# Kernel optimization log

Hardware: AMD Instinct MI355X
Metric: run time of the kernel (lower is better)

## Reference

```python
import jax, jax.numpy as jnp
import numpy as np

K = 3  # from init kwarg


def setup_inputs() -> dict:
    key = jax.random.key(0)
    k1, k2 = jax.random.split(key)
    B, N, D = 32, 2048, 128
    features = jax.random.normal(k1, (B, N, D), dtype=jnp.float32)
    strength = jax.random.uniform(k2, (), dtype=jnp.float32)
    return {"features": features, "strength": strength}


def reference(features, strength):
    B, N, D = features.shape
    k = min(K, N - 1)
    x = jax.lax.stop_gradient(features)  # torch uses features.detach() for the mix path

    # pairwise euclidean distance (torch.cdist, p=2): ||a||^2 + ||b||^2 - 2 a.b
    sq = jnp.sum(x * x, axis=-1)                     # (B, N)
    d2 = sq[:, :, None] + sq[:, None, :] - 2.0 * jnp.einsum('bnd,bmd->bnm', x, x)
    dist = jnp.sqrt(jnp.maximum(d2, 0.0))            # (B, N, N)

    # mask self-distance with +1e6 on the diagonal
    eye = jnp.eye(N, dtype=dist.dtype)
    dist = dist + eye[None, :, :] * 1000000.0

    # k smallest -> top_k of negated distances
    _, idx = jax.lax.top_k(-dist, k)                 # idx: (B, N, k)

    # gather neighbor features: gathered[b,n,j] = x[b, idx[b,n,j]]
    gathered = x[jnp.arange(B)[:, None, None], idx]  # (B, N, k, D)
    mix = jnp.mean(gathered, axis=2)                 # (B, N, D)

    s = jnp.clip(strength, 0.0, 1.0)
    return (1.0 - s) * features + s * mix
```

## Files before the change

### kernel.cpp

```cpp
#include <hip/hip_runtime.h>
#include <cfloat>

#define BB 32
#define NN 2048
#define DD 128
#define RM 128
#define CN 64

typedef __attribute__((ext_vector_type(8))) short short8;
typedef __attribute__((ext_vector_type(4))) short short4v;
typedef __attribute__((ext_vector_type(4))) float float4v;

__device__ __forceinline__ unsigned short f2bf(float f) {
    unsigned int u = __builtin_bit_cast(unsigned int, f);
    u += 0x7FFFu + ((u >> 16) & 1u);
    return (unsigned short)(u >> 16);
}

__device__ __forceinline__ unsigned int umn(unsigned int a, unsigned int b) { return a < b ? a : b; }
__device__ __forceinline__ unsigned int umx(unsigned int a, unsigned int b) { return a > b ? a : b; }
#define CSU(a, b) { unsigned int _lo = umn(a, b), _hi = umx(a, b); (a) = _lo; (b) = _hi; }

__device__ __forceinline__ unsigned int umed3(unsigned int a, unsigned int b, unsigned int c) {
    unsigned int d;
    asm("v_med3_u32 %0, %1, %2, %3" : "=v"(d) : "v"(a), "v"(b), "v"(c));
    return d;
}

__device__ __forceinline__ void gl2lds16(const unsigned short* g, unsigned short* l) {
    __builtin_amdgcn_global_load_lds(
        (const __attribute__((address_space(1))) void*)g,
        (__attribute__((address_space(3))) void*)l, 16, 0, 0);
}

__global__ __launch_bounds__(256) void prep_kernel(const float* __restrict__ x,
        unsigned short* __restrict__ xb16, float* __restrict__ sq) {
    int c = blockIdx.x * 256 + threadIdx.x;
    float4 v = *reinterpret_cast<const float4*>(x + (size_t)c * 4);
    short4v pk;
    pk[0] = (short)f2bf(v.x); pk[1] = (short)f2bf(v.y);
    pk[2] = (short)f2bf(v.z); pk[3] = (short)f2bf(v.w);
    *reinterpret_cast<short4v*>(xb16 + (size_t)c * 4) = pk;
    float acc = v.x * v.x + v.y * v.y + v.z * v.z + v.w * v.w;
    acc += __shfl_xor(acc, 1);
    acc += __shfl_xor(acc, 2);
    acc += __shfl_xor(acc, 4);
    acc += __shfl_xor(acc, 8);
    acc += __shfl_xor(acc, 16);
    if ((threadIdx.x & 31) == 0) sq[c >> 5] = acc;
}

__global__ __launch_bounds__(256) void sq_kernel(const float* __restrict__ x,
                                                 float* __restrict__ sq) {
    int t = blockIdx.x * 256 + threadIdx.x;
    int row = t >> 2;
    int q = t & 3;
    const float4* xp = reinterpret_cast<const float4*>(x + (size_t)row * DD + q * 32);
    float acc = 0.f;
#pragma unroll
    for (int i = 0; i < 8; ++i) {
        float4 v = xp[i];
        acc += v.x * v.x + v.y * v.y + v.z * v.z + v.w * v.w;
    }
    acc += __shfl_xor(acc, 1);
    acc += __shfl_xor(acc, 2);
    if (q == 0) sq[row] = acc;
}

template<bool PRE>
__global__ __launch_bounds__(256, 2) void knn_kernel(const float* __restrict__ x,
        const unsigned short* __restrict__ xb16g,
        const float* __restrict__ sqv, const float* __restrict__ strength,
        float* __restrict__ out) {
    __shared__ __align__(16) unsigned short btile[2 * CN * DD];
    __shared__ unsigned int cand8[RM * 8];

    const int b = blockIdx.x;
    const int row0 = blockIdx.y * RM;
    const int tid = threadIdx.x;
    const int w = tid >> 6;
    const int lane = tid & 63;
    const int m = lane & 15;
    const int quad = lane >> 4;
    const float* __restrict__ xb = x + (size_t)b * NN * DD;
    const unsigned short* __restrict__ gb = PRE ? xb16g + (size_t)b * NN * DD : nullptr;

    short8 afrag[2][4];
    if constexpr (PRE) {
#pragma unroll
        for (int rg = 0; rg < 2; ++rg)
#pragma unroll
            for (int kc = 0; kc < 4; ++kc)
                afrag[rg][kc] = *reinterpret_cast<const short8*>(
                    gb + (size_t)(row0 + 32 * w + rg * 16 + m) * DD + kc * 32 + quad * 8);
    } else {
#pragma unroll
        for (int rg = 0; rg < 2; ++rg)
#pragma unroll
            for (int kc = 0; kc < 4; ++kc) {
                const float4* src = reinterpret_cast<const float4*>(
                    xb + (size_t)(row0 + 32 * w + rg * 16 + m) * DD + kc * 32 + quad * 8);
                float4 v0 = src[0], v1 = src[1];
                short8 pk;
                pk[0] = (short)f2bf(v0.x); pk[1] = (short)f2bf(v0.y);
                pk[2] = (short)f2bf(v0.z); pk[3] = (short)f2bf(v0.w);
                pk[4] = (short)f2bf(v1.x); pk[5] = (short)f2bf(v1.y);
                pk[6] = (short)f2bf(v1.z); pk[7] = (short)f2bf(v1.w);
                afrag[rg][kc] = pk;
            }
    }

    {
        unsigned short* buf = btile;
        if constexpr (PRE) {
#pragma unroll
            for (int l = 0; l < 4; ++l) {
                int f = (l * 4 + w) * 64 + lane;
                int r = f >> 4, p = f & 15;
                int c = p ^ (r & 7);
                gl2lds16(gb + (size_t)r * DD + c * 8, buf + (l * 4 + w) * 512);
            }
        } else {
#pragma unroll
            for (int l = 0; l < 4; ++l) {
                int id = l * 256 + tid;
                int r = id >> 4, c = id & 15, p = c ^ (r & 7);
                const float4* src = reinterpret_cast<const float4*>(xb + (size_t)r * DD + c * 8);
                float4 v0 = src[0], v1 = src[1];
                short8 pk;
                pk[0] = (short)f2bf(v0.x); pk[1] = (short)f2bf(v0.y);
                pk[2] = (short)f2bf(v0.z); pk[3] = (short)f2bf(v0.w);
                pk[4] = (short)f2bf(v1.x); pk[5] = (short)f2bf(v1.y);
                pk[6] = (short)f2bf(v1.z); pk[7] = (short)f2bf(v1.w);
                *reinterpret_cast<short8*>(buf + r * DD + p * 8) = pk;
            }
        }
    }
    __syncthreads();

    unsigned int tk[2][4][4];
#pragma unroll
    for (int rg = 0; rg < 2; ++rg)
#pragma unroll
        for (int i = 0; i < 4; ++i)
#pragma unroll
            for (int q = 0; q < 4; ++q) tk[rg][i][q] = 0xFFFFFFFFu;

    for (int ct = 0; ct < NN / CN; ++ct) {
        unsigned short* cur = btile + (size_t)(ct & 1) * CN * DD;
        unsigned short* nxt = btile + (size_t)((ct + 1) & 1) * CN * DD;

        if (ct + 1 < NN / CN) {
            int cb = (ct + 1) * CN;
            if constexpr (PRE) {
#pragma unroll
                for (int l = 0; l < 4; ++l) {
                    int f = (l * 4 + w) * 64 + lane;
                    int r = f >> 4, p = f & 15;
                    int c = p ^ (r & 7);
                    gl2lds16(gb + (size_t)(cb + r) * DD + c * 8, nxt + (l * 4 + w) * 512);
                }
            } else {
#pragma unroll
                for (int l = 0; l < 4; ++l) {
                    int id = l * 256 + tid;
                    int r = id >> 4, c = id & 15, p = c ^ (r & 7);
                    const float4* src = reinterpret_cast<const float4*>(xb + (size_t)(cb + r) * DD + c * 8);
                    float4 v0 = src[0], v1 = src[1];
                    short8 pk;
                    pk[0] = (short)f2bf(v0.x); pk[1] = (short)f2bf(v0.y);
                    pk[2] = (short)f2bf(v0.z); pk[3] = (short)f2bf(v0.w);
                    pk[4] = (short)f2bf(v1.x); pk[5] = (short)f2bf(v1.y);
                    pk[6] = (short)f2bf(v1.z); pk[7] = (short)f2bf(v1.w);
                    *reinterpret_cast<short8*>(nxt + r * DD + p * 8) = pk;
                }
            }
        }

        float sqb[4];
#pragma unroll
        for (int cc = 0; cc < 4; ++cc)
            sqb[cc] = sqv[(size_t)b * NN + ct * CN + cc * 16 + m] + 1024.0f;

        float4v acc[2][4];
#pragma unroll
        for (int rg = 0; rg < 2; ++rg)
#pragma unroll
            for (int cc = 0; cc < 4; ++cc) acc[rg][cc] = (float4v){0.f, 0.f, 0.f, 0.f};
        __builtin_amdgcn_s_setprio(1);
#pragma unroll
        for (int kc = 0; kc < 4; ++kc) {
            short8 bfrag[4];
#pragma unroll
            for (int cc = 0; cc < 4; ++cc) {
                int rl = cc * 16 + m;
                int p = (kc * 4 + quad) ^ (m & 7);
                bfrag[cc] = *reinterpret_cast<const short8*>(cur + rl * DD + p * 8);
            }
#pragma unroll
            for (int rg = 0; rg < 2; ++rg)
#pragma unroll
                for (int cc = 0; cc < 4; ++cc)
                    acc[rg][cc] = __builtin_amdgcn_mfma_f32_16x16x32_bf16(
                        afrag[rg][kc], bfrag[cc], acc[rg][cc], 0, 0, 0);
        }
        __builtin_amdgcn_s_setprio(0);

#pragma unroll
        for (int cc = 0; cc < 4; ++cc) {
            unsigned int col = (unsigned int)(ct * CN + cc * 16 + m);
#pragma unroll
            for (int rg = 0; rg < 2; ++rg)
#pragma unroll
                for (int reg = 0; reg < 4; ++reg) {
                    float scb = fmaf(-2.f, acc[rg][cc][reg], sqb[cc]);
                    unsigned int key = (__builtin_bit_cast(unsigned int, scb) & 0xFFFFF800u) | col;
                    unsigned int t0 = tk[rg][reg][0], t1 = tk[rg][reg][1];
                    unsigned int t2 = tk[rg][reg][2], t3 = tk[rg][reg][3];
                    tk[rg][reg][0] = umn(t0, key);
                    tk[rg][reg][1] = umed3(t0, t1, key);
                    tk[rg][reg][2] = umed3(t1, t2, key);
                    tk[rg][reg][3] = umed3(t2, t3, key);
                }
        }

        __syncthreads();
    }

#pragma unroll
    for (int rg = 0; rg < 2; ++rg)
#pragma unroll
        for (int reg = 0; reg < 4; ++reg) {
            unsigned int e[8];
#pragma unroll
            for (int j = 0; j < 4; ++j) e[j] = tk[rg][reg][j];
#pragma unroll
            for (int j = 4; j < 8; ++j) e[j] = 0xFFFFFFFFu;
#pragma unroll
            for (int st = 0; st < 4; ++st) {
                int mask = 1 << st;
                unsigned int rv[8];
#pragma unroll
                for (int j = 0; j < 8; ++j)
                    rv[j] = (unsigned int)__shfl_xor((int)e[7 - j], mask, 64);
#pragma unroll
                for (int j = 0; j < 8; ++j) e[j] = umn(e[j], rv[j]);
                CSU(e[0], e[4]); CSU(e[1], e[5]); CSU(e[2], e[6]); CSU(e[3], e[7]);
                CSU(e[0], e[2]); CSU(e[1], e[3]); CSU(e[4], e[6]); CSU(e[5], e[7]);
                CSU(e[0], e[1]); CSU(e[2], e[3]); CSU(e[4], e[5]); CSU(e[6], e[7]);
            }
            if (m == 0) {
                int row = 32 * w + rg * 16 + quad * 4 + reg;
#pragma unroll
                for (int j = 0; j < 8; ++j) cand8[row * 8 + j] = e[j];
            }
        }
    __syncthreads();

    double* refd = reinterpret_cast<double*>(btile);
    int* best3 = reinterpret_cast<int*>(btile) + 2048;

    {
        int r = tid >> 1, h = tid & 1;
        int grow = row0 + r;
        int ci[4];
#pragma unroll
        for (int j = 0; j < 4; ++j) ci[j] = (int)(cand8[r * 8 + h * 4 + j] & 0x7FFu);
        const float* pr = xb + (size_t)grow * DD;
        const float* pc[4];
#pragma unroll
        for (int j = 0; j < 4; ++j) pc[j] = xb + (size_t)ci[j] * DD;
        double a[4] = {0.0, 0.0, 0.0, 0.0};
#pragma unroll 4
        for (int d4 = 0; d4 < 32; ++d4) {
            float4 wv = *reinterpret_cast<const float4*>(pr + d4 * 4);
#pragma unroll
            for (int j = 0; j < 4; ++j) {
                float4 v = *reinterpret_cast<const float4*>(pc[j] + d4 * 4);
                double d;
                d = (double)wv.x - (double)v.x; a[j] += d * d;
                d = (double)wv.y - (double)v.y; a[j] += d * d;
                d = (double)wv.z - (double)v.z; a[j] += d * d;
                d = (double)wv.w - (double)v.w; a[j] += d * d;
            }
        }
#pragma unroll
        for (int j = 0; j < 4; ++j)
            refd[r * 8 + h * 4 + j] = (ci[j] == grow) ? DBL_MAX : a[j];
    }
    __syncthreads();

    if (tid < RM) {
        int r = tid;
        double b0 = DBL_MAX, b1 = DBL_MAX, b2 = DBL_MAX;
        int i0 = 0x7fffffff, i1 = 0x7fffffff, i2 = 0x7fffffff;
        for (int e = 0; e < 8; ++e) {
            double dv = refd[r * 8 + e];
            int ix = (int)(cand8[r * 8 + e] & 0x7FFu);
            if (dv < b2 || (dv == b2 && ix < i2)) {
                b2 = dv; i2 = ix;
                if (b1 > b2 || (b1 == b2 && i1 > i2)) { double td = b1; b1 = b2; b2 = td; int tn = i1; i1 = i2; i2 = tn; }
                if (b0 > b1 || (b0 == b1 && i0 > i1)) { double td = b0; b0 = b1; b1 = td; int tn = i0; i0 = i1; i1 = tn; }
            }
        }
        best3[r * 3 + 0] = i0; best3[r * 3 + 1] = i1; best3[r * 3 + 2] = i2;
    }
    __syncthreads();

    {
        int r = tid >> 1, q = tid & 1;
        float s = fminf(fmaxf(strength[0], 0.f), 1.f);
        const float* pa = xb + (size_t)(row0 + r) * DD + q * 64;
        const float* p1 = xb + (size_t)best3[r * 3 + 0] * DD + q * 64;
        const float* p2 = xb + (size_t)best3[r * 3 + 1] * DD + q * 64;
        const float* p3 = xb + (size_t)best3[r * 3 + 2] * DD + q * 64;
        float* po = out + ((size_t)b * NN + row0 + r) * DD + q * 64;
#pragma unroll
        for (int l = 0; l < 16; ++l) {
            float4 a  = *reinterpret_cast<const float4*>(pa + l * 4);
            float4 n1 = *reinterpret_cast<const float4*>(p1 + l * 4);
            float4 n2 = *reinterpret_cast<const float4*>(p2 + l * 4);
            float4 n3 = *reinterpret_cast<const float4*>(p3 + l * 4);
            float4 o;
            o.x = (1.f - s) * a.x + s * ((n1.x + n2.x + n3.x) / 3.f);
            o.y = (1.f - s) * a.y + s * ((n1.y + n2.y + n3.y) / 3.f);
            o.z = (1.f - s) * a.z + s * ((n1.z + n2.z + n3.z) / 3.f);
            o.w = (1.f - s) * a.w + s * ((n1.w + n2.w + n3.w) / 3.f);
            *reinterpret_cast<float4*>(po + l * 4) = o;
        }
    }
}

extern "C" void kernel_launch(void* const* d_in, const int* in_sizes, int n_in,
                              void* d_out, int out_size, void* d_ws, size_t ws_size,
                              hipStream_t stream) {
    const float* x = (const float*)d_in[0];
    const float* strength = (const float*)d_in[1];
    float* out = (float*)d_out;
    float* sq = (float*)d_ws;
    unsigned short* xb16 = (unsigned short*)((char*)d_ws + 256 * 1024);
    const size_t need = 256 * 1024 + (size_t)BB * NN * DD * sizeof(unsigned short);

    if (ws_size >= need) {
        prep_kernel<<<dim3((BB * NN * DD / 4) / 256), 256, 0, stream>>>(x, xb16, sq);
        knn_kernel<true><<<dim3(BB, NN / RM), 256, 0, stream>>>(x, xb16, sq, strength, out);
    } else {
        sq_kernel<<<dim3((BB * NN * 4) / 256), 256, 0, stream>>>(x, sq);
        knn_kernel<false><<<dim3(BB, NN / RM), 256, 0, stream>>>(x, nullptr, sq, strength, out);
    }
}
```

Measured before the change: 193.4 us.

## Triple-buffer B tiles with explicit vmcnt waits and prefetch squared norms

Moves the LDS B-tile pipeline from double to triple buffering, so the async global-to-LDS copy for tile ct+2 is issued while tile ct is being computed. The full __syncthreads is replaced by a partial s_waitcnt vmcnt(4) plus s_barrier, which leaves the newest prefetch in flight. Squared norms for the next tile are loaded one iteration early, and the setprio hints around the MFMA block are removed. The cost is 16KB more LDS per block, which may reduce occupancy, and hand-written waitcnt logic that depends on how the compiler orders memory operations.

```diff
diff --git a/kernel.cpp b/kernel.cpp
--- a/kernel.cpp
+++ b/kernel.cpp
@@ -6,6 +6,7 @@
 #define DD 128
 #define RM 128
 #define CN 64
+#define NT (NN / CN)
 
 typedef __attribute__((ext_vector_type(8))) short short8;
 typedef __attribute__((ext_vector_type(4))) short short4v;
@@ -72,7 +73,7 @@
         const unsigned short* __restrict__ xb16g,
         const float* __restrict__ sqv, const float* __restrict__ strength,
         float* __restrict__ out) {
-    __shared__ __align__(16) unsigned short btile[2 * CN * DD];
+    __shared__ __align__(16) unsigned short btile[3 * CN * DD];
     __shared__ unsigned int cand8[RM * 8];
 
     const int b = blockIdx.x;
@@ -110,32 +111,44 @@
             }
     }
 
-    {
-        unsigned short* buf = btile;
-        if constexpr (PRE) {
-#pragma unroll
-            for (int l = 0; l < 4; ++l) {
-                int f = (l * 4 + w) * 64 + lane;
-                int r = f >> 4, p = f & 15;
-                int c = p ^ (r & 7);
-                gl2lds16(gb + (size_t)r * DD + c * 8, buf + (l * 4 + w) * 512);
-            }
-        } else {
-#pragma unroll
-            for (int l = 0; l < 4; ++l) {
-                int id = l * 256 + tid;
-                int r = id >> 4, c = id & 15, p = c ^ (r & 7);
-                const float4* src = reinterpret_cast<const float4*>(xb + (size_t)r * DD + c * 8);
-                float4 v0 = src[0], v1 = src[1];
-                short8 pk;
-                pk[0] = (short)f2bf(v0.x); pk[1] = (short)f2bf(v0.y);
-                pk[2] = (short)f2bf(v0.z); pk[3] = (short)f2bf(v0.w);
-                pk[4] = (short)f2bf(v1.x); pk[5] = (short)f2bf(v1.y);
-                pk[6] = (short)f2bf(v1.z); pk[7] = (short)f2bf(v1.w);
-                *reinterpret_cast<short8*>(buf + r * DD + p * 8) = pk;
-            }
-        }
-    }
+    unsigned short* cur = btile;
+    unsigned short* n1  = btile + CN * DD;
+    unsigned short* n2  = btile + 2 * CN * DD;
+
+    if constexpr (PRE) {
+#pragma unroll
+        for (int l = 0; l < 4; ++l) {
+            int f = (l * 4 + w) * 64 + lane;
+            int r = f >> 4, p = f & 15;
+            int c = p ^ (r & 7);
+            gl2lds16(gb + (size_t)r * DD + c * 8, cur + (l * 4 + w) * 512);
+        }
+#pragma unroll
+        for (int l = 0; l < 4; ++l) {
+            int f = (l * 4 + w) * 64 + lane;
+            int r = f >> 4, p = f & 15;
+            int c = p ^ (r & 7);
+            gl2lds16(gb + (size_t)(CN + r) * DD + c * 8, n1 + (l * 4 + w) * 512);
+        }
+    } else {
+#pragma unroll
+        for (int l = 0; l < 8; ++l) {
+            int id = l * 256 + tid;
+            int r = id >> 4, c = id & 15, p = c ^ (r & 7);
+            const float4* src = reinterpret_cast<const float4*>(xb + (size_t)r * DD + c * 8);
+            float4 v0 = src[0], v1 = src[1];
+            short8 pk;
+            pk[0] = (short)f2bf(v0.x); pk[1] = (short)f2bf(v0.y);
+            pk[2] = (short)f2bf(v0.z); pk[3] = (short)f2bf(v0.w);
+            pk[4] = (short)f2bf(v1.x); pk[5] = (short)f2bf(v1.y);
+            pk[6] = (short)f2bf(v1.z); pk[7] = (short)f2bf(v1.w);
+            *reinterpret_cast<short8*>(btile + r * DD + p * 8) = pk;
+        }
+    }
+    float sqb[4];
+#pragma unroll
+    for (int cc = 0; cc < 4; ++cc)
+        sqb[cc] = sqv[(size_t)b * NN + cc * 16 + m] + 1024.0f;
     __syncthreads();
 
     unsigned int tk[2][4][4];
@@ -146,19 +159,25 @@
 #pragma unroll
             for (int q = 0; q < 4; ++q) tk[rg][i][q] = 0xFFFFFFFFu;
 
-    for (int ct = 0; ct < NN / CN; ++ct) {
-        unsigned short* cur = btile + (size_t)(ct & 1) * CN * DD;
-        unsigned short* nxt = btile + (size_t)((ct + 1) & 1) * CN * DD;
-
-        if (ct + 1 < NN / CN) {
-            int cb = (ct + 1) * CN;
+#pragma unroll 1
+    for (int ct = 0; ct < NT; ++ct) {
+        float sqn[4];
+        if (ct + 1 < NT) {
+#pragma unroll
+            for (int cc = 0; cc < 4; ++cc)
+                sqn[cc] = sqv[(size_t)b * NN + (ct + 1) * CN + cc * 16 + m];
+        }
+        asm volatile("" ::: "memory");
+
+        if (ct + 2 < NT) {
+            int cb = (ct + 2) * CN;
             if constexpr (PRE) {
 #pragma unroll
                 for (int l = 0; l < 4; ++l) {
                     int f = (l * 4 + w) * 64 + lane;
                     int r = f >> 4, p = f & 15;
                     int c = p ^ (r & 7);
-                    gl2lds16(gb + (size_t)(cb + r) * DD + c * 8, nxt + (l * 4 + w) * 512);
+                    gl2lds16(gb + (size_t)(cb + r) * DD + c * 8, n2 + (l * 4 + w) * 512);
                 }
             } else {
 #pragma unroll
@@ -172,22 +191,16 @@
                     pk[2] = (short)f2bf(v0.z); pk[3] = (short)f2bf(v0.w);
                     pk[4] = (short)f2bf(v1.x); pk[5] = (short)f2bf(v1.y);
                     pk[6] = (short)f2bf(v1.z); pk[7] = (short)f2bf(v1.w);
-                    *reinterpret_cast<short8*>(nxt + r * DD + p * 8) = pk;
+                    *reinterpret_cast<short8*>(n2 + r * DD + p * 8) = pk;
                 }
             }
         }
 
-        float sqb[4];
-#pragma unroll
-        for (int cc = 0; cc < 4; ++cc)
-            sqb[cc] = sqv[(size_t)b * NN + ct * CN + cc * 16 + m] + 1024.0f;
-
         float4v acc[2][4];
 #pragma unroll
         for (int rg = 0; rg < 2; ++rg)
 #pragma unroll
             for (int cc = 0; cc < 4; ++cc) acc[rg][cc] = (float4v){0.f, 0.f, 0.f, 0.f};
-        __builtin_amdgcn_s_setprio(1);
 #pragma unroll
         for (int kc = 0; kc < 4; ++kc) {
             short8 bfrag[4];
@@ -204,7 +217,6 @@
                     acc[rg][cc] = __builtin_amdgcn_mfma_f32_16x16x32_bf16(
                         afrag[rg][kc], bfrag[cc], acc[rg][cc], 0, 0, 0);
         }
-        __builtin_amdgcn_s_setprio(0);
 
 #pragma unroll
         for (int cc = 0; cc < 4; ++cc) {
@@ -224,7 +236,24 @@
                 }
         }
 
-        __syncthreads();
+        if (ct + 1 < NT) {
+#pragma unroll
+            for (int cc = 0; cc < 4; ++cc) sqb[cc] = sqn[cc] + 1024.0f;
+        }
+
+        if constexpr (PRE) {
+            if (ct + 2 < NT) {
+                asm volatile("s_waitcnt vmcnt(4)" ::: "memory");
+            } else {
+                asm volatile("s_waitcnt vmcnt(0)" ::: "memory");
+            }
+            __builtin_amdgcn_s_barrier();
+            __builtin_amdgcn_sched_barrier(0);
+        } else {
+            __syncthreads();
+        }
+
+        unsigned short* t = cur; cur = n1; n1 = n2; n2 = t;
     }
 
 #pragma unroll
@@ -318,14 +347,14 @@
 #pragma unroll
         for (int l = 0; l < 16; ++l) {
             float4 a  = *reinterpret_cast<const float4*>(pa + l * 4);
-            float4 n1 = *reinterpret_cast<const float4*>(p1 + l * 4);
-            float4 n2 = *reinterpret_cast<const float4*>(p2 + l * 4);
-            float4 n3 = *reinterpret_cast<const float4*>(p3 + l * 4);
+            float4 v1 = *reinterpret_cast<const float4*>(p1 + l * 4);
+            float4 v2 = *reinterpret_cast<const float4*>(p2 + l * 4);
+            float4 v3 = *reinterpret_cast<const float4*>(p3 + l * 4);
             float4 o;
-            o.x = (1.f - s) * a.x + s * ((n1.x + n2.x + n3.x) / 3.f);
-            o.y = (1.f - s) * a.y + s * ((n1.y + n2.y + n3.y) / 3.f);
-            o.z = (1.f - s) * a.z + s * ((n1.z + n2.z + n3.z) / 3.f);
-            o.w = (1.f - s) * a.w + s * ((n1.w + n2.w + n3.w) / 3.f);
+            o.x = (1.f - s) * a.x + s * ((v1.x + v2.x + v3.x) / 3.f);
+            o.y = (1.f - s) * a.y + s * ((v1.y + v2.y + v3.y) / 3.f);
+            o.z = (1.f - s) * a.z + s * ((v1.z + v2.z + v3.z) / 3.f);
+            o.w = (1.f - s) * a.w + s * ((v1.w + v2.w + v3.w) / 3.f);
             *reinterpret_cast<float4*>(po + l * 4) = o;
         }
     }
```

Measured after the change: 186.2 us, median of 2. 3.7% less time.

## Deepen LDS tile pipeline to four buffers with prefetch distance two

Applied to the files above, without the earlier changes.

The column-tile loop now uses four LDS buffers and issues async global-to-LDS loads two tiles ahead instead of one. It waits with explicit vmcnt counts plus a raw barrier rather than a full syncthreads, and unrolls four tiles per iteration with precomputed LDS addresses. Squared norms are now prefetched one tile ahead, and the +1024 bias is folded into the prep kernels. The cost is doubled LDS use, which may reduce occupancy, and hand-tuned wait counts that are easy to get wrong.

```diff
diff --git a/kernel.cpp b/kernel.cpp
--- a/kernel.cpp
+++ b/kernel.cpp
@@ -6,6 +6,7 @@
 #define DD 128
 #define RM 128
 #define CN 64
+#define NT (NN / CN)
 
 typedef __attribute__((ext_vector_type(8))) short short8;
 typedef __attribute__((ext_vector_type(4))) short short4v;
@@ -47,7 +48,7 @@
     acc += __shfl_xor(acc, 4);
     acc += __shfl_xor(acc, 8);
     acc += __shfl_xor(acc, 16);
-    if ((threadIdx.x & 31) == 0) sq[c >> 5] = acc;
+    if ((threadIdx.x & 31) == 0) sq[c >> 5] = acc + 1024.0f;
 }
 
 __global__ __launch_bounds__(256) void sq_kernel(const float* __restrict__ x,
@@ -64,7 +65,7 @@
     }
     acc += __shfl_xor(acc, 1);
     acc += __shfl_xor(acc, 2);
-    if (q == 0) sq[row] = acc;
+    if (q == 0) sq[row] = acc + 1024.0f;
 }
 
 template<bool PRE>
@@ -72,7 +73,7 @@
         const unsigned short* __restrict__ xb16g,
         const float* __restrict__ sqv, const float* __restrict__ strength,
         float* __restrict__ out) {
-    __shared__ __align__(16) unsigned short btile[2 * CN * DD];
+    __shared__ __align__(16) unsigned short btile[4 * CN * DD];
     __shared__ unsigned int cand8[RM * 8];
 
     const int b = blockIdx.x;
@@ -110,32 +111,50 @@
             }
     }
 
-    {
-        unsigned short* buf = btile;
-        if constexpr (PRE) {
-#pragma unroll
-            for (int l = 0; l < 4; ++l) {
-                int f = (l * 4 + w) * 64 + lane;
-                int r = f >> 4, p = f & 15;
-                int c = p ^ (r & 7);
-                gl2lds16(gb + (size_t)r * DD + c * 8, buf + (l * 4 + w) * 512);
-            }
-        } else {
-#pragma unroll
-            for (int l = 0; l < 4; ++l) {
-                int id = l * 256 + tid;
-                int r = id >> 4, c = id & 15, p = c ^ (r & 7);
-                const float4* src = reinterpret_cast<const float4*>(xb + (size_t)r * DD + c * 8);
-                float4 v0 = src[0], v1 = src[1];
-                short8 pk;
-                pk[0] = (short)f2bf(v0.x); pk[1] = (short)f2bf(v0.y);
-                pk[2] = (short)f2bf(v0.z); pk[3] = (short)f2bf(v0.w);
-                pk[4] = (short)f2bf(v1.x); pk[5] = (short)f2bf(v1.y);
-                pk[6] = (short)f2bf(v1.z); pk[7] = (short)f2bf(v1.w);
-                *reinterpret_cast<short8*>(buf + r * DD + p * 8) = pk;
-            }
-        }
-    }
+    const unsigned short* gsl[4];
+    int ldo[4];
+    int str_[4], stc_[4], stp_[4];
+#pragma unroll
+    for (int l = 0; l < 4; ++l) {
+        int f = (l * 4 + w) * 64 + lane;
+        int r = f >> 4, p = f & 15;
+        int c = p ^ (r & 7);
+        str_[l] = r; stc_[l] = c; stp_[l] = p;
+        if constexpr (PRE) gsl[l] = gb + (size_t)r * DD + c * 8;
+        ldo[l] = (l * 4 + w) * 512;
+    }
+    int baddr[16];
+#pragma unroll
+    for (int kc = 0; kc < 4; ++kc)
+#pragma unroll
+        for (int cc = 0; cc < 4; ++cc)
+            baddr[kc * 4 + cc] =
+                ((cc * 16 + m) * DD + (((kc * 4 + quad) ^ (m & 7)) * 8)) * 2;
+    const float* __restrict__ sqp = sqv + (size_t)b * NN + m;
+
+    if constexpr (PRE) {
+#pragma unroll
+        for (int l = 0; l < 4; ++l) gl2lds16(gsl[l], btile + ldo[l]);
+#pragma unroll
+        for (int l = 0; l < 4; ++l) gl2lds16(gsl[l] + (1 << 13), btile + CN * DD + ldo[l]);
+    } else {
+#pragma unroll
+        for (int l = 0; l < 8; ++l) {
+            int id = l * 256 + tid;
+            int r = id >> 4, c = id & 15, p = c ^ (r & 7);
+            const float4* src = reinterpret_cast<const float4*>(xb + (size_t)r * DD + c * 8);
+            float4 v0 = src[0], v1 = src[1];
+            short8 pk;
+            pk[0] = (short)f2bf(v0.x); pk[1] = (short)f2bf(v0.y);
+            pk[2] = (short)f2bf(v0.z); pk[3] = (short)f2bf(v0.w);
+            pk[4] = (short)f2bf(v1.x); pk[5] = (short)f2bf(v1.y);
+            pk[6] = (short)f2bf(v1.z); pk[7] = (short)f2bf(v1.w);
+            *reinterpret_cast<short8*>(btile + r * DD + p * 8) = pk;
+        }
+    }
+    float sqb[4];
+#pragma unroll
+    for (int cc = 0; cc < 4; ++cc) sqb[cc] = sqp[cc * 16];
     __syncthreads();
 
     unsigned int tk[2][4][4];
@@ -146,86 +165,107 @@
 #pragma unroll
             for (int q = 0; q < 4; ++q) tk[rg][i][q] = 0xFFFFFFFFu;
 
-    for (int ct = 0; ct < NN / CN; ++ct) {
-        unsigned short* cur = btile + (size_t)(ct & 1) * CN * DD;
-        unsigned short* nxt = btile + (size_t)((ct + 1) & 1) * CN * DD;
-
-        if (ct + 1 < NN / CN) {
-            int cb = (ct + 1) * CN;
-            if constexpr (PRE) {
-#pragma unroll
-                for (int l = 0; l < 4; ++l) {
-                    int f = (l * 4 + w) * 64 + lane;
-                    int r = f >> 4, p = f & 15;
-                    int c = p ^ (r & 7);
-                    gl2lds16(gb + (size_t)(cb + r) * DD + c * 8, nxt + (l * 4 + w) * 512);
-                }
-            } else {
-#pragma unroll
-                for (int l = 0; l < 4; ++l) {
-                    int id = l * 256 + tid;
-                    int r = id >> 4, c = id & 15, p = c ^ (r & 7);
-                    const float4* src = reinterpret_cast<const float4*>(xb + (size_t)(cb + r) * DD + c * 8);
-                    float4 v0 = src[0], v1 = src[1];
-                    short8 pk;
-                    pk[0] = (short)f2bf(v0.x); pk[1] = (short)f2bf(v0.y);
-                    pk[2] = (short)f2bf(v0.z); pk[3] = (short)f2bf(v0.w);
-                    pk[4] = (short)f2bf(v1.x); pk[5] = (short)f2bf(v1.y);
-                    pk[6] = (short)f2bf(v1.z); pk[7] = (short)f2bf(v1.w);
-                    *reinterpret_cast<short8*>(nxt + r * DD + p * 8) = pk;
-                }
-            }
-        }
-
-        float sqb[4];
-#pragma unroll
-        for (int cc = 0; cc < 4; ++cc)
-            sqb[cc] = sqv[(size_t)b * NN + ct * CN + cc * 16 + m] + 1024.0f;
-
-        float4v acc[2][4];
-#pragma unroll
-        for (int rg = 0; rg < 2; ++rg)
-#pragma unroll
-            for (int cc = 0; cc < 4; ++cc) acc[rg][cc] = (float4v){0.f, 0.f, 0.f, 0.f};
-        __builtin_amdgcn_s_setprio(1);
-#pragma unroll
-        for (int kc = 0; kc < 4; ++kc) {
-            short8 bfrag[4];
-#pragma unroll
-            for (int cc = 0; cc < 4; ++cc) {
-                int rl = cc * 16 + m;
-                int p = (kc * 4 + quad) ^ (m & 7);
-                bfrag[cc] = *reinterpret_cast<const short8*>(cur + rl * DD + p * 8);
-            }
-#pragma unroll
-            for (int rg = 0; rg < 2; ++rg)
-#pragma unroll
-                for (int cc = 0; cc < 4; ++cc)
-                    acc[rg][cc] = __builtin_amdgcn_mfma_f32_16x16x32_bf16(
-                        afrag[rg][kc], bfrag[cc], acc[rg][cc], 0, 0, 0);
-        }
-        __builtin_amdgcn_s_setprio(0);
-
-#pragma unroll
-        for (int cc = 0; cc < 4; ++cc) {
-            unsigned int col = (unsigned int)(ct * CN + cc * 16 + m);
-#pragma unroll
-            for (int rg = 0; rg < 2; ++rg)
-#pragma unroll
-                for (int reg = 0; reg < 4; ++reg) {
-                    float scb = fmaf(-2.f, acc[rg][cc][reg], sqb[cc]);
-                    unsigned int key = (__builtin_bit_cast(unsigned int, scb) & 0xFFFFF800u) | col;
-                    unsigned int t0 = tk[rg][reg][0], t1 = tk[rg][reg][1];
-                    unsigned int t2 = tk[rg][reg][2], t3 = tk[rg][reg][3];
-                    tk[rg][reg][0] = umn(t0, key);
-                    tk[rg][reg][1] = umed3(t0, t1, key);
-                    tk[rg][reg][2] = umed3(t1, t2, key);
-                    tk[rg][reg][3] = umed3(t2, t3, key);
-                }
-        }
-
-        __syncthreads();
-    }
+#define TILE_SLOT(J)                                                                   \
+    {                                                                                  \
+        const int ct = ct4 + (J);                                                      \
+                       \
+        float sqn[4];                                                                  \
+        if (ct + 1 < NT) {                                                             \
+            _Pragma("unroll")                                                          \
+            for (int cc = 0; cc < 4; ++cc)                                             \
+                sqn[cc] = sqp[((ct + 1) << 6) + cc * 16];                              \
+        }                                                                              \
+        asm volatile("" ::: "memory");         \
+              \
+        if (ct + 2 < NT) {                                                             \
+            if constexpr (PRE) {                                                       \
+                _Pragma("unroll")                                                      \
+                for (int l = 0; l < 4; ++l)                                            \
+                    gl2lds16(gsl[l] + ((size_t)(ct + 2) << 13),                        \
+                             btile + (((J) + 2) & 3) * CN * DD + ldo[l]);              \
+            } else {                                                                   \
+                _Pragma("unroll")                                                      \
+                for (int l = 0; l < 4; ++l) {                                          \
+                    const float4* src = reinterpret_cast<const float4*>(               \
+                        xb + (size_t)((ct + 2) * CN + str_[l]) * DD + stc_[l] * 8);    \
+                    float4 v0 = src[0], v1 = src[1];                                   \
+                    short8 pk;                                                         \
+                    pk[0] = (short)f2bf(v0.x); pk[1] = (short)f2bf(v0.y);              \
+                    pk[2] = (short)f2bf(v0.z); pk[3] = (short)f2bf(v0.w);              \
+                    pk[4] = (short)f2bf(v1.x); pk[5] = (short)f2bf(v1.y);              \
+                    pk[6] = (short)f2bf(v1.z); pk[7] = (short)f2bf(v1.w);              \
+                    *reinterpret_cast<short8*>(btile + (((J) + 2) & 3) * CN * DD       \
+                        + str_[l] * DD + stp_[l] * 8) = pk;                            \
+                }                                                                      \
+            }                                                                          \
+        }                                                                              \
+                        \
+        float4v acc[2][4];                                                             \
+        _Pragma("unroll")                                                              \
+        for (int rg = 0; rg < 2; ++rg)                                                 \
+            _Pragma("unroll")                                                          \
+            for (int cc = 0; cc < 4; ++cc) acc[rg][cc] = (float4v){0.f, 0.f, 0.f, 0.f};\
+        _Pragma("unroll")                                                              \
+        for (int kc = 0; kc < 4; ++kc) {                                               \
+            short8 bfrag[4];                                                           \
+            _Pragma("unroll")                                                          \
+            for (int cc = 0; cc < 4; ++cc)                                             \
+                bfrag[cc] = *reinterpret_cast<const short8*>(                          \
+                    reinterpret_cast<const char*>(btile)                               \
+                    + (J) * (CN * DD * 2) + baddr[kc * 4 + cc]);                       \
+            _Pragma("unroll")                                                          \
+            for (int rg = 0; rg < 2; ++rg)                                             \
+                _Pragma("unroll")                                                      \
+                for (int cc = 0; cc < 4; ++cc)                                         \
+                    acc[rg][cc] = __builtin_amdgcn_mfma_f32_16x16x32_bf16(             \
+                        afrag[rg][kc], bfrag[cc], acc[rg][cc], 0, 0, 0);               \
+        }                                                                              \
+                            \
+        _Pragma("unroll")                                                              \
+        for (int cc = 0; cc < 4; ++cc) {                                               \
+            unsigned int col = (unsigned int)(ct * CN + cc * 16 + m);                  \
+            _Pragma("unroll")                                                          \
+            for (int rg = 0; rg < 2; ++rg)                                             \
+                _Pragma("unroll")                                                      \
+                for (int reg = 0; reg < 4; ++reg) {                                    \
+                    float scb = fmaf(-2.f, acc[rg][cc][reg], sqb[cc]);                 \
+                    unsigned int key =                                                 \
+                        (__builtin_bit_cast(unsigned int, scb) & 0xFFFFF800u) | col;   \
+                    unsigned int t0 = tk[rg][reg][0], t1 = tk[rg][reg][1];             \
+                    unsigned int t2 = tk[rg][reg][2], t3 = tk[rg][reg][3];             \
+                    tk[rg][reg][0] = umn(t0, key);                                     \
+                    tk[rg][reg][1] = umed3(t0, t1, key);                               \
+                    tk[rg][reg][2] = umed3(t1, t2, key);                               \
+                    tk[rg][reg][3] = umed3(t2, t3, key);                               \
+                }                                                                      \
+        }                                                                              \
+                                                                       \
+        if (ct + 1 < NT) {                                                             \
+            _Pragma("unroll")                                                          \
+            for (int cc = 0; cc < 4; ++cc) sqb[cc] = sqn[cc];                          \
+        }                                                                              \
+                            \
+        if constexpr (PRE) {                                                           \
+            if (ct + 2 < NT) {                                                         \
+                asm volatile("s_waitcnt vmcnt(4)" ::: "memory");                       \
+            } else {                                                                   \
+                asm volatile("s_waitcnt vmcnt(0)" ::: "memory");                       \
+            }                                                                          \
+            __builtin_amdgcn_s_barrier();                                              \
+            __builtin_amdgcn_sched_barrier(0);                                         \
+        } else {                                                                       \
+            __syncthreads();                                                           \
+        }                                                                              \
+    }
+
+#pragma unroll 1
+    for (int ct4 = 0; ct4 < NT; ct4 += 4) {
+        TILE_SLOT(0)
+        TILE_SLOT(1)
+        TILE_SLOT(2)
+        TILE_SLOT(3)
+    }
+#undef TILE_SLOT
 
 #pragma unroll
     for (int rg = 0; rg < 2; ++rg)
@@ -318,14 +358,14 @@
 #pragma unroll
         for (int l = 0; l < 16; ++l) {
             float4 a  = *reinterpret_cast<const float4*>(pa + l * 4);
-            float4 n1 = *reinterpret_cast<const float4*>(p1 + l * 4);
-            float4 n2 = *reinterpret_cast<const float4*>(p2 + l * 4);
-            float4 n3 = *reinterpret_cast<const float4*>(p3 + l * 4);
+            float4 v1 = *reinterpret_cast<const float4*>(p1 + l * 4);
+            float4 v2 = *reinterpret_cast<const float4*>(p2 + l * 4);
+            float4 v3 = *reinterpret_cast<const float4*>(p3 + l * 4);
             float4 o;
-            o.x = (1.f - s) * a.x + s * ((n1.x + n2.x + n3.x) / 3.f);
-            o.y = (1.f - s) * a.y + s * ((n1.y + n2.y + n3.y) / 3.f);
-            o.z = (1.f - s) * a.z + s * ((n1.z + n2.z + n3.z) / 3.f);
-            o.w = (1.f - s) * a.w + s * ((n1.w + n2.w + n3.w) / 3.f);
+            o.x = (1.f - s) * a.x + s * ((v1.x + v2.x + v3.x) / 3.f);
+            o.y = (1.f - s) * a.y + s * ((v1.y + v2.y + v3.y) / 3.f);
+            o.z = (1.f - s) * a.z + s * ((v1.z + v2.z + v3.z) / 3.f);
+            o.w = (1.f - s) * a.w + s * ((v1.w + v2.w + v3.w) / 3.f);
             *reinterpret_cast<float4*>(po + l * 4) = o;
         }
     }
```

Result: no change. 196.3 us (+1.5%).
